# Performance work log

Measured on AMD Instinct MI355X. Metric: run time of the kernel, lower is better.

## Reference

```python
import jax, jax.numpy as jnp
import numpy as np

DK = 64  # head dim = n_features // n_heads = 512 // 8


def setup_inputs() -> dict:
    key = jax.random.key(0)
    ks = jax.random.split(key, 6)
    B, N, D = 2, 4096, 512
    feature = jax.random.normal(ks[0], (B, N, D), dtype=jnp.float32)
    Sh = jax.random.normal(ks[1], (B, N, N), dtype=jnp.float32)
    Sw = jax.random.normal(ks[2], (B, N, N), dtype=jnp.float32)
    # torch Linear weights are [out, in]; xavier-uniform init
    lim = np.sqrt(6.0 / (D + DK)).astype(np.float32)
    wq_w = jax.random.uniform(ks[3], (DK, D), jnp.float32, -lim, lim)
    wk_w = jax.random.uniform(ks[4], (DK, D), jnp.float32, -lim, lim)
    wv_w = jax.random.uniform(ks[5], (DK, D), jnp.float32, -lim, lim)
    zb = jnp.zeros((DK,), jnp.float32)
    return {"feature": feature, "Sh": Sh, "Sw": Sw,
            "wq_w": wq_w, "wq_b": zb, "wk_w": wk_w, "wk_b": zb,
            "wv_w": wv_w, "wv_b": zb}


def reference(feature, Sh, Sw, wq_w, wq_b, wk_w, wk_b, wv_w, wv_b):
    # Linear projections (torch: x @ W.T + b)
    Q = jnp.einsum('bnd,kd->bnk', feature, wq_w) + wq_b  # [B,N,dk]
    K = jnp.einsum('bnd,kd->bnk', feature, wk_w) + wk_b  # [B,N,dk]
    V = jnp.einsum('bnd,kd->bnk', feature, wv_w) + wv_b  # [B,N,dv]
    sqrt_dk = jnp.sqrt(jnp.float32(Q.shape[-1]))
    # scores = (QK^T + Sh + Sw) / sqrt(dk)  -- biases added BEFORE scaling,
    # exactly as in attnFunc
    A = (jnp.einsum('bqk,bnk->bqn', Q, K) + Sh + Sw) / sqrt_dk  # [B,N,N]
    A = jax.nn.softmax(A, axis=-1)
    return jnp.einsum('bqn,bnk->bqk', A, V)  # [B,N,dv]
```

## Files before the change

kernel.cpp:

```cpp
#include <hip/hip_runtime.h>
#include <hip/hip_bf16.h>


typedef short bf16x8 __attribute__((ext_vector_type(8)));
typedef short bf16x4 __attribute__((ext_vector_type(4)));
typedef float f32x4  __attribute__((ext_vector_type(4)));

#if __has_builtin(__builtin_amdgcn_exp2f)
#define EXP2F(x) __builtin_amdgcn_exp2f(x)
#else
#define EXP2F(x) exp2f(x)
#endif
#if __has_builtin(__builtin_amdgcn_rcpf)
#define RCPF(x) __builtin_amdgcn_rcpf(x)
#else
#define RCPF(x) (1.0f / (x))
#endif

__device__ __forceinline__ f32x4 mfma16(bf16x8 a, bf16x8 b, f32x4 c) {
  return __builtin_amdgcn_mfma_f32_16x16x32_bf16(a, b, c, 0, 0, 0);
}
__device__ __forceinline__ short f2b(float x) {
  __hip_bfloat16 h = __float2bfloat16(x);
  return __builtin_bit_cast(short, h);
}
__device__ __forceinline__ float b2f(short s) {
  return __bfloat162float(__builtin_bit_cast(__hip_bfloat16, s));
}
__device__ __forceinline__ void split_hl(float x, short& h, short& l) {
  __hip_bfloat16 bh = __float2bfloat16(x);
  h = __builtin_bit_cast(short, bh);
  l = f2b(x - __bfloat162float(bh));
}

__global__ void wcvt_kernel(const float* __restrict__ wq, const float* __restrict__ wk,
                            const float* __restrict__ wv,
                            short* __restrict__ wh, short* __restrict__ wl) {
  int idx = (blockIdx.x * 256 + threadIdx.x) * 4;
  int p = idx >> 15;
  int off = idx & 32767;
  const float* src = (p == 0) ? wq : (p == 1) ? wk : wv;
  f32x4 v = *(const f32x4*)(src + off);
  bf16x4 h, l;
#pragma unroll
  for (int j = 0; j < 4; ++j) { short hh, ll; split_hl(v[j], hh, ll); h[j] = hh; l[j] = ll; }
  *(bf16x4*)(wh + p * 32768 + off) = h;
  *(bf16x4*)(wl + p * 32768 + off) = l;
}

__global__ __launch_bounds__(256) void proj_kernel(
    const float* __restrict__ feat, const short* __restrict__ wh, const short* __restrict__ wl,
    const float* __restrict__ bq, const float* __restrict__ bk, const float* __restrict__ bv,
    short* __restrict__ Qh, short* __restrict__ Ql,
    short* __restrict__ Kh, short* __restrict__ Kl, short* __restrict__ Vt) {
  const int lane = threadIdx.x & 63, wave = threadIdx.x >> 6;
  const int lq = lane & 15, quad = lane >> 4;
  const int wid = blockIdx.x * 4 + wave;
  const int p = wid >> 9, rg = wid & 511;
  const int rbase = rg * 16;
  const float Cs = 0.18033688011112042f;

  f32x4 acc[4];
#pragma unroll
  for (int t = 0; t < 4; ++t) acc[t] = (f32x4){0.f, 0.f, 0.f, 0.f};

  const float* frow = feat + (size_t)(rbase + lq) * 512 + quad * 8;
  const int wrow = p * 64;
  for (int ks = 0; ks < 16; ++ks) {
    f32x4 f0 = *(const f32x4*)(frow + ks * 32);
    f32x4 f1 = *(const f32x4*)(frow + ks * 32 + 4);
    bf16x8 fh, fl;
#pragma unroll
    for (int j = 0; j < 4; ++j) {
      short hh, ll;
      split_hl(f0[j], hh, ll); fh[j] = hh; fl[j] = ll;
      split_hl(f1[j], hh, ll); fh[j + 4] = hh; fl[j + 4] = ll;
    }
#pragma unroll
    for (int t = 0; t < 4; ++t) {
      const int wo = (wrow + t * 16 + lq) * 512 + ks * 32 + quad * 8;
      bf16x8 wfh = *(const bf16x8*)(wh + wo);
      bf16x8 wfl = *(const bf16x8*)(wl + wo);
      acc[t] = mfma16(fh, wfh, acc[t]);
      acc[t] = mfma16(fl, wfh, acc[t]);
      acc[t] = mfma16(fh, wfl, acc[t]);
    }
  }
  const int b = rbase >> 12, rloc = rbase & 4095;
  if (p == 0) {
#pragma unroll
    for (int t = 0; t < 4; ++t) {
      const int dk = t * 16 + lq;
      const float bb = bq[dk];
#pragma unroll
      for (int r = 0; r < 4; ++r) {
        const int row = rbase + 4 * quad + r;
        short h, l;
        split_hl((acc[t][r] + bb) * Cs, h, l);
        Qh[row * 64 + dk] = h; Ql[row * 64 + dk] = l;
      }
    }
  } else if (p == 1) {
#pragma unroll
    for (int t = 0; t < 4; ++t) {
      const int dk = t * 16 + lq;
      const float bb = bk[dk];
#pragma unroll
      for (int r = 0; r < 4; ++r) {
        const int row = rbase + 4 * quad + r;
        short h, l;
        split_hl(acc[t][r] + bb, h, l);
        Kh[row * 64 + dk] = h; Kl[row * 64 + dk] = l;
      }
    }
  } else {
#pragma unroll
    for (int t = 0; t < 4; ++t) {
      const int dk = t * 16 + lq;
      const float bb = bv[dk];
      bf16x4 vpack;
#pragma unroll
      for (int r = 0; r < 4; ++r) vpack[r] = f2b(acc[t][r] + bb);
      *(bf16x4*)(Vt + (size_t)(b * 64 + dk) * 4096 + rloc + 4 * quad) = vpack;
    }
  }
}

__global__ __launch_bounds__(256) void bias_prep_kernel(
    const float* __restrict__ Sh, const float* __restrict__ Sw,
    short* __restrict__ BiasBf) {
  const float Cs = 0.18033688011112042f;
  const int g = blockIdx.x * 256 + threadIdx.x;
#pragma unroll
  for (int it = 0; it < 16; it += 4) {
    f32x4 a[4], c[4];
#pragma unroll
    for (int j = 0; j < 4; ++j) {
      const size_t o = ((size_t)(it + j) * 524288 + g) * 4;
      a[j] = __builtin_nontemporal_load((const f32x4*)(Sh + o));
      c[j] = __builtin_nontemporal_load((const f32x4*)(Sw + o));
    }
#pragma unroll
    for (int j = 0; j < 4; ++j) {
      const size_t o = ((size_t)(it + j) * 524288 + g) * 4;
      f32x4 s = (a[j] + c[j]) * Cs;
      bf16x4 pk;
#pragma unroll
      for (int r = 0; r < 4; ++r) pk[r] = f2b(s[r]);
      *(bf16x4*)(BiasBf + o) = pk;
    }
  }
}

__global__ __launch_bounds__(256, 4) void attn_kernel(
    const short* __restrict__ BiasBf,
    const short* __restrict__ Qh, const short* __restrict__ Ql,
    const short* __restrict__ Kh, const short* __restrict__ Vt,
    float* __restrict__ Opart, float* __restrict__ lpart) {
  __shared__ short Plds[4][16][40];
  const int bid = blockIdx.x;
  const int sp = bid & 7, qt = (bid >> 3) & 63, b = bid >> 9;
  const int tid = threadIdx.x;
  const int wave = tid >> 6, lane = tid & 63, lq = lane & 15, quad = lane >> 4;
  const int qbase = qt * 64 + wave * 16;

  const int qidx = (b * 4096 + qbase + lq) * 64 + quad * 8;
  const bf16x8 qfh0 = *(const bf16x8*)(Qh + qidx);
  const bf16x8 qfh1 = *(const bf16x8*)(Qh + qidx + 32);
  const bf16x8 qfl0 = *(const bf16x8*)(Ql + qidx);
  const bf16x8 qfl1 = *(const bf16x8*)(Ql + qidx + 32);

  const short* brow = BiasBf + (size_t)(b * 4096 + qbase + lq) * 4096 + sp * 512;

  f32x4 accO[4];
#pragma unroll
  for (int u = 0; u < 4; ++u) accO[u] = (f32x4){0.f, 0.f, 0.f, 0.f};
  float lsum = 0.f;
  short* pw_ = &Plds[wave][0][0];
  const short* vbase = Vt + (size_t)b * 64 * 4096;

#pragma unroll 2
  for (int it = 0; it < 16; ++it) {
    const int kb = sp * 512 + it * 32;
    bf16x8 kh0[2], kh1[2];
#pragma unroll
    for (int t = 0; t < 2; ++t) {
      const int kidx = (b * 4096 + kb + t * 16 + lq) * 64 + quad * 8;
      kh0[t] = *(const bf16x8*)(Kh + kidx);
      kh1[t] = *(const bf16x8*)(Kh + kidx + 32);
    }
    bf16x8 vf[4];
#pragma unroll
    for (int u = 0; u < 4; ++u)
      vf[u] = *(const bf16x8*)(vbase + (size_t)(u * 16 + lq) * 4096 + kb + quad * 8);
    const bf16x4 bb0 = *(const bf16x4*)(brow + it * 32 + 4 * quad);
    const bf16x4 bb1 = *(const bf16x4*)(brow + it * 32 + 16 + 4 * quad);

    f32x4 accS[2];
#pragma unroll
    for (int t = 0; t < 2; ++t) accS[t] = (f32x4){0.f, 0.f, 0.f, 0.f};
#pragma unroll
    for (int t = 0; t < 2; ++t) {
      accS[t] = mfma16(kh0[t], qfh0, accS[t]);
      accS[t] = mfma16(kh1[t], qfh1, accS[t]);
      accS[t] = mfma16(kh0[t], qfl0, accS[t]);
      accS[t] = mfma16(kh1[t], qfl1, accS[t]);
    }

#pragma unroll
    for (int t = 0; t < 2; ++t) {
      const bf16x4 bb = t ? bb1 : bb0;
      bf16x4 pk;
#pragma unroll
      for (int r = 0; r < 4; ++r) {
        float s = accS[t][r] + b2f(bb[r]);
        float p = EXP2F(s);
        lsum += p;
        pk[r] = f2b(p);
      }
      *(bf16x4*)(pw_ + lq * 40 + 16 * t + 4 * quad) = pk;
    }

    const bf16x8 pa = *(const bf16x8*)(pw_ + lq * 40 + quad * 8);
#pragma unroll
    for (int u = 0; u < 4; ++u) accO[u] = mfma16(pa, vf[u], accO[u]);
  }

  lsum += __shfl_xor(lsum, 16, 64);
  lsum += __shfl_xor(lsum, 32, 64);

  const int orowW = sp * 8192 + b * 4096 + qbase;
  if (quad == 0) lpart[orowW + lq] = lsum;
#pragma unroll
  for (int u = 0; u < 4; ++u)
#pragma unroll
    for (int r = 0; r < 4; ++r)
      Opart[(size_t)(orowW + 4 * quad + r) * 64 + u * 16 + lq] = accO[u][r];
}

__global__ void combine_kernel(const float* __restrict__ Opart, const float* __restrict__ lpart,
                               float* __restrict__ out) {
  const int g = blockIdx.x * 256 + threadIdx.x;
  const int row = g >> 4;
  f32x4 o = (f32x4){0.f, 0.f, 0.f, 0.f};
  float l = 0.f;
#pragma unroll
  for (int s = 0; s < 8; ++s) {
    o += __builtin_nontemporal_load((const f32x4*)(Opart + (size_t)s * 524288 + g * 4));
    l += lpart[s * 8192 + row];
  }
  const float rl = RCPF(l);
  *(f32x4*)(out + g * 4) = o * rl;
}

extern "C" void kernel_launch(void* const* d_in, const int* in_sizes, int n_in,
                              void* d_out, int out_size, void* d_ws, size_t ws_size,
                              hipStream_t stream) {
  const float* feature = (const float*)d_in[0];
  const float* Sh = (const float*)d_in[1];
  const float* Sw = (const float*)d_in[2];
  const float* wq = (const float*)d_in[3];
  const float* bq = (const float*)d_in[4];
  const float* wk = (const float*)d_in[5];
  const float* bk = (const float*)d_in[6];
  const float* wv = (const float*)d_in[7];
  const float* bv = (const float*)d_in[8];

  char* ws = (char*)d_ws;
  const size_t MB = 1u << 20;
  short* Qh = (short*)(ws + 0 * MB);
  short* Ql = (short*)(ws + 1 * MB);
  short* Kh = (short*)(ws + 2 * MB);
  short* Kl = (short*)(ws + 3 * MB);
  short* Vt = (short*)(ws + 4 * MB);
  short* wh = (short*)(ws + 5 * MB);
  short* wl = (short*)(ws + 5 * MB + 262144);
  float* lpart = (float*)(ws + 5 * MB + 524288);
  float* Opart = (float*)(ws + 6 * MB);
  short* BiasBf = (short*)(ws + 24 * MB);

  wcvt_kernel<<<96, 256, 0, stream>>>(wq, wk, wv, wh, wl);
  proj_kernel<<<384, 256, 0, stream>>>(feature, wh, wl, bq, bk, bv, Qh, Ql, Kh, Kl, Vt);
  bias_prep_kernel<<<2048, 256, 0, stream>>>(Sh, Sw, BiasBf);
  attn_kernel<<<1024, 256, 0, stream>>>(BiasBf, Qh, Ql, Kh, Vt, Opart, lpart);
  combine_kernel<<<512, 256, 0, stream>>>(Opart, lpart, (float*)d_out);
}
```

Measured before the change: 398.2 us.

## Fuse bias preparation into attention kernel via shared-memory bias tile

```diff
diff --git a/kernel.cpp b/kernel.cpp
--- a/kernel.cpp
+++ b/kernel.cpp
@@ -126,52 +126,56 @@
   }
 }
 
-__global__ __launch_bounds__(256) void bias_prep_kernel(
+__global__ __launch_bounds__(256, 2) void attn_kernel(
     const float* __restrict__ Sh, const float* __restrict__ Sw,
-    short* __restrict__ BiasBf) {
-  const float Cs = 0.18033688011112042f;
-  const int g = blockIdx.x * 256 + threadIdx.x;
-#pragma unroll
-  for (int it = 0; it < 16; it += 4) {
-    f32x4 a[4], c[4];
-#pragma unroll
-    for (int j = 0; j < 4; ++j) {
-      const size_t o = ((size_t)(it + j) * 524288 + g) * 4;
-      a[j] = __builtin_nontemporal_load((const f32x4*)(Sh + o));
-      c[j] = __builtin_nontemporal_load((const f32x4*)(Sw + o));
-    }
-#pragma unroll
-    for (int j = 0; j < 4; ++j) {
-      const size_t o = ((size_t)(it + j) * 524288 + g) * 4;
-      f32x4 s = (a[j] + c[j]) * Cs;
-      bf16x4 pk;
-#pragma unroll
-      for (int r = 0; r < 4; ++r) pk[r] = f2b(s[r]);
-      *(bf16x4*)(BiasBf + o) = pk;
-    }
-  }
-}
-
-__global__ __launch_bounds__(256, 4) void attn_kernel(
-    const short* __restrict__ BiasBf,
     const short* __restrict__ Qh, const short* __restrict__ Ql,
     const short* __restrict__ Kh, const short* __restrict__ Vt,
     float* __restrict__ Opart, float* __restrict__ lpart) {
+  __shared__ short BiasL[16][2056];
   __shared__ short Plds[4][16][40];
   const int bid = blockIdx.x;
-  const int sp = bid & 7, qt = (bid >> 3) & 63, b = bid >> 9;
+  const int half = bid & 1, Rg = bid >> 1;
+  const int R = Rg * 16;
+  const int b = R >> 12;
   const int tid = threadIdx.x;
   const int wave = tid >> 6, lane = tid & 63, lq = lane & 15, quad = lane >> 4;
-  const int qbase = qt * 64 + wave * 16;
-
-  const int qidx = (b * 4096 + qbase + lq) * 64 + quad * 8;
+  const float Cs = 0.18033688011112042f;
+
+  {
+    const float* shp = Sh + (size_t)(R + 4 * wave) * 4096 + half * 2048 + lane * 4;
+    const float* swp = Sw + (size_t)(R + 4 * wave) * 4096 + half * 2048 + lane * 4;
+    short* bl = &BiasL[4 * wave][0];
+    f32x4 ra[8], rc[8];
+#pragma unroll
+    for (int p = 0; p < 8; ++p) {
+      const size_t off = (size_t)(p >> 3) * 4096 + (p & 7) * 256;
+      ra[p] = __builtin_nontemporal_load((const f32x4*)(shp + off));
+      rc[p] = __builtin_nontemporal_load((const f32x4*)(swp + off));
+    }
+#pragma unroll
+    for (int p = 0; p < 32; ++p) {
+      const int sl = p & 7;
+      f32x4 s = (ra[sl] + rc[sl]) * Cs;
+      bf16x4 pk;
+#pragma unroll
+      for (int j = 0; j < 4; ++j) pk[j] = f2b(s[j]);
+      *(bf16x4*)(bl + (p >> 3) * 2056 + (p & 7) * 256 + lane * 4) = pk;
+      if (p + 8 < 32) {
+        const int pn = p + 8;
+        const size_t off = (size_t)(pn >> 3) * 4096 + (pn & 7) * 256;
+        ra[sl] = __builtin_nontemporal_load((const f32x4*)(shp + off));
+        rc[sl] = __builtin_nontemporal_load((const f32x4*)(swp + off));
+      }
+    }
+  }
+  __syncthreads();
+
+  const int qidx = (R + lq) * 64 + quad * 8;
   const bf16x8 qfh0 = *(const bf16x8*)(Qh + qidx);
   const bf16x8 qfh1 = *(const bf16x8*)(Qh + qidx + 32);
   const bf16x8 qfl0 = *(const bf16x8*)(Ql + qidx);
   const bf16x8 qfl1 = *(const bf16x8*)(Ql + qidx + 32);
 
-  const short* brow = BiasBf + (size_t)(b * 4096 + qbase + lq) * 4096 + sp * 512;
-
   f32x4 accO[4];
 #pragma unroll
   for (int u = 0; u < 4; ++u) accO[u] = (f32x4){0.f, 0.f, 0.f, 0.f};
@@ -181,7 +185,8 @@
 
 #pragma unroll 2
   for (int it = 0; it < 16; ++it) {
-    const int kb = sp * 512 + it * 32;
+    const int kl = wave * 512 + it * 32;
+    const int kb = half * 2048 + kl;
     bf16x8 kh0[2], kh1[2];
 #pragma unroll
     for (int t = 0; t < 2; ++t) {
@@ -193,8 +198,6 @@
 #pragma unroll
     for (int u = 0; u < 4; ++u)
       vf[u] = *(const bf16x8*)(vbase + (size_t)(u * 16 + lq) * 4096 + kb + quad * 8);
-    const bf16x4 bb0 = *(const bf16x4*)(brow + it * 32 + 4 * quad);
-    const bf16x4 bb1 = *(const bf16x4*)(brow + it * 32 + 16 + 4 * quad);
 
     f32x4 accS[2];
 #pragma unroll
@@ -209,7 +212,7 @@
 
 #pragma unroll
     for (int t = 0; t < 2; ++t) {
-      const bf16x4 bb = t ? bb1 : bb0;
+      const bf16x4 bb = *(const bf16x4*)(&BiasL[lq][kl + 16 * t + 4 * quad]);
       bf16x4 pk;
 #pragma unroll
       for (int r = 0; r < 4; ++r) {
@@ -229,7 +232,8 @@
   lsum += __shfl_xor(lsum, 16, 64);
   lsum += __shfl_xor(lsum, 32, 64);
 
-  const int orowW = sp * 8192 + b * 4096 + qbase;
+  const int sp = half * 4 + wave;
+  const int orowW = sp * 8192 + R;
   if (quad == 0) lpart[orowW + lq] = lsum;
 #pragma unroll
   for (int u = 0; u < 4; ++u)
@@ -277,11 +281,9 @@
   short* wl = (short*)(ws + 5 * MB + 262144);
   float* lpart = (float*)(ws + 5 * MB + 524288);
   float* Opart = (float*)(ws + 6 * MB);
-  short* BiasBf = (short*)(ws + 24 * MB);
 
   wcvt_kernel<<<96, 256, 0, stream>>>(wq, wk, wv, wh, wl);
   proj_kernel<<<384, 256, 0, stream>>>(feature, wh, wl, bq, bk, bv, Qh, Ql, Kh, Kl, Vt);
-  bias_prep_kernel<<<2048, 256, 0, stream>>>(Sh, Sw, BiasBf);
-  attn_kernel<<<1024, 256, 0, stream>>>(BiasBf, Qh, Ql, Kh, Vt, Opart, lpart);
+  attn_kernel<<<1024, 256, 0, stream>>>(Sh, Sw, Qh, Ql, Kh, Vt, Opart, lpart);
   combine_kernel<<<512, 256, 0, stream>>>(Opart, lpart, (float*)d_out);
 }
```

New measurement: 365.9 us. -8.1%, faster.
